# Kernel optimization log

Measured on AMD Instinct MI355X. Metric: run time of the kernel, lower is better.

Reference implementation:

```python
import jax, jax.numpy as jnp
import numpy as np

N_NODES = 300000
DIM = 64
NNZ = 4800000


def setup_inputs() -> dict:
    key = jax.random.key(0)
    ks = jax.random.split(key, 8)
    emb_all = 0.1 * jax.random.normal(ks[0], (N_NODES, DIM), dtype=jnp.float32)
    # edge values ~ symmetric-normalized adjacency scale (avg degree 16 -> ~1/16)
    vals = jax.random.uniform(ks[1], (NNZ,), dtype=jnp.float32) * (1.0 / 16.0)
    vals2 = jax.random.uniform(ks[2], (NNZ,), dtype=jnp.float32) * (1.0 / 16.0)
    rows = jnp.sort(jax.random.randint(ks[3], (NNZ,), 0, N_NODES, dtype=jnp.int32))
    cols = jax.random.randint(ks[4], (NNZ,), 0, N_NODES, dtype=jnp.int32)
    rows2 = jnp.sort(jax.random.randint(ks[5], (NNZ,), 0, N_NODES, dtype=jnp.int32))
    cols2 = jax.random.randint(ks[6], (NNZ,), 0, N_NODES, dtype=jnp.int32)
    return {
        "emb_all": emb_all,
        "vals": vals,
        "vals2": vals2,
        "rows": rows,
        "cols": cols,
        "rows2": rows2,
        "cols2": cols2,
        "n_layers": 3,
        "num_users": 100000,
    }


def _spmm(rows, cols, vals, x, n):
    # sparse [n,n] @ dense [n,d] via gather + segment-sum
    return jax.ops.segment_sum(vals[:, None] * x[cols], rows, num_segments=n)


def _pearson(x, y):
    # per-row pearson correlation over the last (latent) dim -> [N]
    xd = x - jnp.mean(x, axis=-1, keepdims=True)
    yd = y - jnp.mean(y, axis=-1, keepdims=True)
    num = jnp.sum(xd * yd, axis=-1)
    den = jnp.sqrt(jnp.sum(xd * xd, axis=-1)) * jnp.sqrt(jnp.sum(yd * yd, axis=-1))
    den = jnp.where(den < 1e-7, jnp.float32(1e-7), den)
    return num / den


def reference(emb_all, vals, vals2, rows, cols, rows2, cols2, n_layers, num_users):
    n = emb_all.shape[0]
    e0 = emb_all
    embs2 = [e0]
    # layer 0: plain LightGCN propagation on G
    e = _spmm(rows, cols, vals, e0, n)
    embs2.append(e)
    # layers 1..n_layers: pearson-gated propagation on G2
    for _ in range(n_layers):
        b = _pearson(embs2[-1], e0)  # [N]
        prop = _spmm(rows2, cols2, vals2, embs2[-1], n)
        e = b[:, None] * prop + (1.0 - b)[:, None] * e0
        embs2.append(e)
    light_out = jnp.mean(jnp.stack(embs2, axis=1), axis=1)  # [N, d]
    users = light_out[:num_users]
    items = light_out[num_users:]
    return users, items
```

## Files before the change

### kernel.cpp

```cpp
#include <hip/hip_runtime.h>

#define DIM 64

typedef __attribute__((ext_vector_type(4))) float f4;
typedef __attribute__((ext_vector_type(2))) float f2;
typedef __attribute__((ext_vector_type(4))) unsigned int u4;
typedef __attribute__((ext_vector_type(2))) unsigned int u2;

#define SEL_LO 0x01000504u
#define SEL_HI 0x03020706u
#define ONE2   0x3f803f80u

__device__ __forceinline__ float bflo(unsigned u) { return __uint_as_float(u << 16); }
__device__ __forceinline__ float bfhi(unsigned u) { return __uint_as_float(u & 0xffff0000u); }
__device__ __forceinline__ unsigned bfr(float f) {
    unsigned u = __float_as_uint(f);
    return (u + 0x7fffu + ((u >> 16) & 1u)) >> 16;
}
__device__ __forceinline__ unsigned packbf(float e, float o) { return bfr(e) | (bfr(o) << 16); }
__device__ __forceinline__ unsigned cvtpk(float lo, float hi) {
    unsigned r;
    asm("v_cvt_pk_bf16_f32 %0, %1, %2" : "=v"(r) : "v"(lo), "v"(hi));
    return r;
}
__device__ __forceinline__ float dot2bf(unsigned a, unsigned b, float c) {
    float d;
    asm("v_dot2_f32_bf16 %0, %1, %2, %3" : "=v"(d) : "v"(a), "v"(b), "v"(c));
    return d;
}
__device__ __forceinline__ float gsum8(float v) {
    v += __shfl_xor(v, 1, 64);
    v += __shfl_xor(v, 2, 64);
    v += __shfl_xor(v, 4, 64);
    return v;
}

__global__ void build_row_ptr_kernel(const int* __restrict__ rows, int nnz,
                                     int n, int* __restrict__ row_ptr) {
    int r = blockIdx.x * blockDim.x + threadIdx.x;
    if (r > n) return;
    int lo = 0, hi = nnz;
    while (lo < hi) {
        int mid = (lo + hi) >> 1;
        if (rows[mid] < r) lo = mid + 1; else hi = mid;
    }
    row_ptr[r] = lo;
}

__global__ void cvt_bf16_kernel(const float* __restrict__ in,
                                unsigned int* __restrict__ out, int n8) {
    int i = blockIdx.x * blockDim.x + threadIdx.x;
    if (i >= n8) return;
    const f4* p = (const f4*)in + 2 * (size_t)i;
    f4 a = p[0], b = p[1];
    u4 o;
    o.x = packbf(a.x, a.y); o.y = packbf(a.z, a.w);
    o.z = packbf(b.x, b.y); o.w = packbf(b.z, b.w);
    ((u4*)out)[i] = o;
}

template <int MODE>
__global__ __launch_bounds__(256) void layer_kernel(
    const float* __restrict__ emb,
    const unsigned short* __restrict__ t0,
    const unsigned short* __restrict__ eprev,
    const float* __restrict__ vals, const int* __restrict__ cols,
    const int* __restrict__ rp, int n,
    unsigned short* __restrict__ enew,
    const unsigned short* __restrict__ e1t,
    const unsigned short* __restrict__ e2t,
    f2* __restrict__ stats,
    float* __restrict__ out)
{
    const int tid  = threadIdx.x;
    const int lane = tid & 63;
    const int j    = lane & 7;
    const int wave = blockIdx.x * (blockDim.x >> 6) + (tid >> 6);
    const int rowg = wave * 8 + (lane >> 3);
    const int rg   = rowg < n ? rowg : n - 1;

    const int start = rp[rg];
    const int end   = rp[rg + 1];
    const int len   = (rowg < n) ? (end - start) : 0;
    const int b0    = start & ~1;
    const int doff  = b0 - start;

    int ml = len;
    ml = max(ml, __shfl_xor(ml, 8, 64));
    ml = max(ml, __shfl_xor(ml, 16, 64));
    ml = max(ml, __shfl_xor(ml, 32, 64));
    const int steps = (ml + 4) >> 2;

    const char* tb8 = (const char*)eprev;
    const unsigned joff = (unsigned)(j << 4);

    float acc[8] = {0.f, 0.f, 0.f, 0.f, 0.f, 0.f, 0.f, 0.f};

    for (int s = 0; s < steps; ++s) {
        const int k = b0 + (s << 2);
        u2 c01 = *(const u2*)(cols + k);
        u2 c23 = *(const u2*)(cols + k + 2);
        f2 v01 = *(const f2*)(vals + k);
        f2 v23 = *(const f2*)(vals + k + 2);
        const int rel = (s << 2) + doff;
        bool ok0 = (unsigned)(rel)     < (unsigned)len;
        bool ok1 = (unsigned)(rel + 1) < (unsigned)len;
        bool ok2 = (unsigned)(rel + 2) < (unsigned)len;
        bool ok3 = (unsigned)(rel + 3) < (unsigned)len;
        unsigned cc0 = ok0 ? (unsigned)c01.x : 0u;
        unsigned cc1 = ok1 ? (unsigned)c01.y : 0u;
        unsigned cc2 = ok2 ? (unsigned)c23.x : 0u;
        unsigned cc3 = ok3 ? (unsigned)c23.y : 0u;
        float w0 = ok0 ? v01.x : 0.f;
        float w1 = ok1 ? v01.y : 0.f;
        float w2 = ok2 ? v23.x : 0.f;
        float w3 = ok3 ? v23.y : 0.f;
        unsigned vp01 = cvtpk(w0, w1);
        unsigned vp23 = cvtpk(w2, w3);
        u4 g0 = *(const u4*)(tb8 + ((cc0 << 7) + joff));
        u4 g1 = *(const u4*)(tb8 + ((cc1 << 7) + joff));
        u4 g2 = *(const u4*)(tb8 + ((cc2 << 7) + joff));
        u4 g3 = *(const u4*)(tb8 + ((cc3 << 7) + joff));
        acc[0] = dot2bf(__builtin_amdgcn_perm(g0.x, g1.x, SEL_LO), vp01, acc[0]);
        acc[1] = dot2bf(__builtin_amdgcn_perm(g0.x, g1.x, SEL_HI), vp01, acc[1]);
        acc[2] = dot2bf(__builtin_amdgcn_perm(g0.y, g1.y, SEL_LO), vp01, acc[2]);
        acc[3] = dot2bf(__builtin_amdgcn_perm(g0.y, g1.y, SEL_HI), vp01, acc[3]);
        acc[4] = dot2bf(__builtin_amdgcn_perm(g0.z, g1.z, SEL_LO), vp01, acc[4]);
        acc[5] = dot2bf(__builtin_amdgcn_perm(g0.z, g1.z, SEL_HI), vp01, acc[5]);
        acc[6] = dot2bf(__builtin_amdgcn_perm(g0.w, g1.w, SEL_LO), vp01, acc[6]);
        acc[7] = dot2bf(__builtin_amdgcn_perm(g0.w, g1.w, SEL_HI), vp01, acc[7]);
        acc[0] = dot2bf(__builtin_amdgcn_perm(g2.x, g3.x, SEL_LO), vp23, acc[0]);
        acc[1] = dot2bf(__builtin_amdgcn_perm(g2.x, g3.x, SEL_HI), vp23, acc[1]);
        acc[2] = dot2bf(__builtin_amdgcn_perm(g2.y, g3.y, SEL_LO), vp23, acc[2]);
        acc[3] = dot2bf(__builtin_amdgcn_perm(g2.y, g3.y, SEL_HI), vp23, acc[3]);
        acc[4] = dot2bf(__builtin_amdgcn_perm(g2.z, g3.z, SEL_LO), vp23, acc[4]);
        acc[5] = dot2bf(__builtin_amdgcn_perm(g2.z, g3.z, SEL_HI), vp23, acc[5]);
        acc[6] = dot2bf(__builtin_amdgcn_perm(g2.w, g3.w, SEL_LO), vp23, acc[6]);
        acc[7] = dot2bf(__builtin_amdgcn_perm(g2.w, g3.w, SEL_HI), vp23, acc[7]);
    }

    const size_t ro = (size_t)rg << 6;

    if (MODE == 0) {
        u4 yr = *((const u4*)(t0 + ro) + j);
        float sy  = dot2bf(yr.x, ONE2,
                    dot2bf(yr.y, ONE2, dot2bf(yr.z, ONE2, dot2bf(yr.w, ONE2, 0.f))));
        float syy = dot2bf(yr.x, yr.x,
                    dot2bf(yr.y, yr.y, dot2bf(yr.z, yr.z, dot2bf(yr.w, yr.w, 0.f))));
        sy = gsum8(sy); syy = gsum8(syy);
        float my  = sy * (1.f / 64.f);
        float vy  = syy - sy * my;
        float svy = sqrtf(fmaxf(vy, 0.f));
        if (rowg < n) {
            if (j == 0) { f2 st; st.x = my; st.y = svy; stats[rowg] = st; }
            u4 o;
            o.x = cvtpk(acc[0], acc[1]); o.y = cvtpk(acc[2], acc[3]);
            o.z = cvtpk(acc[4], acc[5]); o.w = cvtpk(acc[6], acc[7]);
            *((u4*)(enew + ro) + j) = o;
        }
        return;
    }

    u4 xr = *((const u4*)(eprev + ro) + j);
    u4 yr = *((const u4*)(t0 + ro) + j);
    float sx  = dot2bf(xr.x, ONE2,
                dot2bf(xr.y, ONE2, dot2bf(xr.z, ONE2, dot2bf(xr.w, ONE2, 0.f))));
    float sxx = dot2bf(xr.x, xr.x,
                dot2bf(xr.y, xr.y, dot2bf(xr.z, xr.z, dot2bf(xr.w, xr.w, 0.f))));
    float sxy = dot2bf(xr.x, yr.x,
                dot2bf(xr.y, yr.y, dot2bf(xr.z, yr.z, dot2bf(xr.w, yr.w, 0.f))));
    sx = gsum8(sx); sxx = gsum8(sxx); sxy = gsum8(sxy);

    f2 st = stats[rg];
    float mx  = sx * (1.f / 64.f);
    float num = sxy - sx * st.x;
    float vx  = sxx - sx * mx;
    float den = sqrtf(fmaxf(vx, 0.f)) * st.y;
    den = fmaxf(den, 1e-7f);
    float b  = num / den;
    float ob = 1.f - b;

    if (MODE == 1) {
        float y0[8] = { bflo(yr.x), bfhi(yr.x), bflo(yr.y), bfhi(yr.y),
                        bflo(yr.z), bfhi(yr.z), bflo(yr.w), bfhi(yr.w) };
        if (rowg < n) {
            u4 o;
            o.x = cvtpk(b * acc[0] + ob * y0[0], b * acc[1] + ob * y0[1]);
            o.y = cvtpk(b * acc[2] + ob * y0[2], b * acc[3] + ob * y0[3]);
            o.z = cvtpk(b * acc[4] + ob * y0[4], b * acc[5] + ob * y0[5]);
            o.w = cvtpk(b * acc[6] + ob * y0[6], b * acc[7] + ob * y0[7]);
            *((u4*)(enew + ro) + j) = o;
        }
    } else {
        const f4* ep = (const f4*)(emb + ro) + 2 * j;
        f4 ea = ep[0], eb = ep[1];
        float y0[8] = { ea.x, ea.y, ea.z, ea.w, eb.x, eb.y, eb.z, eb.w };
        float xp[8] = { bflo(xr.x), bfhi(xr.x), bflo(xr.y), bfhi(xr.y),
                        bflo(xr.z), bfhi(xr.z), bflo(xr.w), bfhi(xr.w) };
        u4 r1 = *((const u4*)(e1t + ro) + j);
        u4 r2 = *((const u4*)(e2t + ro) + j);
        float s[8];
        s[0] = y0[0] + bflo(r1.x) + bflo(r2.x) + xp[0] + (b * acc[0] + ob * y0[0]);
        s[1] = y0[1] + bfhi(r1.x) + bfhi(r2.x) + xp[1] + (b * acc[1] + ob * y0[1]);
        s[2] = y0[2] + bflo(r1.y) + bflo(r2.y) + xp[2] + (b * acc[2] + ob * y0[2]);
        s[3] = y0[3] + bfhi(r1.y) + bfhi(r2.y) + xp[3] + (b * acc[3] + ob * y0[3]);
        s[4] = y0[4] + bflo(r1.z) + bflo(r2.z) + xp[4] + (b * acc[4] + ob * y0[4]);
        s[5] = y0[5] + bfhi(r1.z) + bfhi(r2.z) + xp[5] + (b * acc[5] + ob * y0[5]);
        s[6] = y0[6] + bflo(r1.w) + bflo(r2.w) + xp[6] + (b * acc[6] + ob * y0[6]);
        s[7] = y0[7] + bfhi(r1.w) + bfhi(r2.w) + xp[7] + (b * acc[7] + ob * y0[7]);
        if (rowg < n) {
            f4 o0 = { s[0] * 0.2f, s[1] * 0.2f, s[2] * 0.2f, s[3] * 0.2f };
            f4 o1 = { s[4] * 0.2f, s[5] * 0.2f, s[6] * 0.2f, s[7] * 0.2f };
            f4* op = (f4*)(out + ro) + 2 * j;
            op[0] = o0; op[1] = o1;
        }
    }
}

extern "C" void kernel_launch(void* const* d_in, const int* in_sizes, int n_in,
                              void* d_out, int out_size, void* d_ws, size_t ws_size,
                              hipStream_t stream) {
    const float* emb   = (const float*)d_in[0];
    const float* vals  = (const float*)d_in[1];
    const float* vals2 = (const float*)d_in[2];
    const int*   rows  = (const int*)d_in[3];
    const int*   cols  = (const int*)d_in[4];
    const int*   rows2 = (const int*)d_in[5];
    const int*   cols2 = (const int*)d_in[6];

    const int n    = in_sizes[0] / DIM;
    const int nnz  = in_sizes[1];
    const int nnz2 = in_sizes[2];

    float* out = (float*)d_out;

    char*  ws       = (char*)d_ws;
    size_t rp_bytes = (((size_t)(n + 1) * sizeof(int)) + 255) & ~(size_t)255;
    size_t st_bytes = (((size_t)n * sizeof(f2)) + 255) & ~(size_t)255;
    size_t tb_bytes = (size_t)n * DIM * sizeof(unsigned short);
    int* rp1 = (int*)ws;
    int* rp2 = (int*)(ws + rp_bytes);
    f2*  ST  = (f2*)(ws + 2 * rp_bytes);
    unsigned short* T0 = (unsigned short*)(ws + 2 * rp_bytes + st_bytes);
    unsigned short* E1 = (unsigned short*)((char*)T0 + tb_bytes);
    unsigned short* E2 = (unsigned short*)((char*)E1 + tb_bytes);
    unsigned short* E3 = (unsigned short*)((char*)E2 + tb_bytes);

    const int tb = 256;
    build_row_ptr_kernel<<<(n + 1 + tb - 1) / tb, tb, 0, stream>>>(rows,  nnz,  n, rp1);
    build_row_ptr_kernel<<<(n + 1 + tb - 1) / tb, tb, 0, stream>>>(rows2, nnz2, n, rp2);

    const int n8 = n * DIM / 8;
    cvt_bf16_kernel<<<(n8 + tb - 1) / tb, tb, 0, stream>>>(emb, (unsigned int*)T0, n8);

    const int waves = (n + 7) / 8;
    const int grid  = (waves + 3) / 4;
    layer_kernel<0><<<grid, tb, 0, stream>>>(emb, T0, T0, vals, cols, rp1, n,
                                             E1, T0, T0, ST, out);
    layer_kernel<1><<<grid, tb, 0, stream>>>(emb, T0, E1, vals2, cols2, rp2, n,
                                             E2, T0, T0, ST, out);
    layer_kernel<1><<<grid, tb, 0, stream>>>(emb, T0, E2, vals2, cols2, rp2, n,
                                             E3, T0, T0, ST, out);
    layer_kernel<2><<<grid, tb, 0, stream>>>(emb, T0, E3, vals2, cols2, rp2, n,
                                             E3, E1, E2, ST, out);
}
```

Before: 496.3 us.

## Precompute next-layer Pearson coefficient in producer epilogue; unroll gather loop to eight edges

Each layer kernel now computes the Pearson gate for the next layer from its freshly written output row and stores it in a small per-row buffer. Consumer kernels then read one float instead of re-reading the previous row and reducing it, which removes a dependent load and a reduction from the epilogue. The edge loop is also unrolled from four to eight edges per step, with eight row gathers in flight, and the cols/vals stream is read with nontemporal loads. The wider unroll raises register pressure and wastes more padded work on short rows.

Result: slower. 509.2 us (+2.6%).

```diff
diff --git a/kernel.cpp b/kernel.cpp
--- a/kernel.cpp
+++ b/kernel.cpp
@@ -69,7 +69,7 @@
     unsigned short* __restrict__ enew,
     const unsigned short* __restrict__ e1t,
     const unsigned short* __restrict__ e2t,
-    f2* __restrict__ stats,
+    f2* __restrict__ stats, float* __restrict__ bbuf,
     float* __restrict__ out)
 {
     const int tid  = threadIdx.x;
@@ -89,60 +89,85 @@
     ml = max(ml, __shfl_xor(ml, 8, 64));
     ml = max(ml, __shfl_xor(ml, 16, 64));
     ml = max(ml, __shfl_xor(ml, 32, 64));
-    const int steps = (ml + 4) >> 2;
+    const int steps = (ml + 8) >> 3;
 
     const char* tb8 = (const char*)eprev;
     const unsigned joff = (unsigned)(j << 4);
+    const size_t ro = (size_t)rg << 6;
+
+    float bcoef = 0.f;
+    if (MODE != 0) bcoef = bbuf[rg];
+    u4 yr = {};
+    if (MODE != 2) yr = *((const u4*)(t0 + ro) + j);
+    f2 st = {};
+    if (MODE == 1) st = stats[rg];
 
     float acc[8] = {0.f, 0.f, 0.f, 0.f, 0.f, 0.f, 0.f, 0.f};
 
     for (int s = 0; s < steps; ++s) {
-        const int k = b0 + (s << 2);
-        u2 c01 = *(const u2*)(cols + k);
-        u2 c23 = *(const u2*)(cols + k + 2);
-        f2 v01 = *(const f2*)(vals + k);
-        f2 v23 = *(const f2*)(vals + k + 2);
-        const int rel = (s << 2) + doff;
+        const int k = b0 + (s << 3);
+        u2 c01 = __builtin_nontemporal_load((const u2*)(cols + k));
+        u2 c23 = __builtin_nontemporal_load((const u2*)(cols + k + 2));
+        u2 c45 = __builtin_nontemporal_load((const u2*)(cols + k + 4));
+        u2 c67 = __builtin_nontemporal_load((const u2*)(cols + k + 6));
+        f2 v01 = __builtin_nontemporal_load((const f2*)(vals + k));
+        f2 v23 = __builtin_nontemporal_load((const f2*)(vals + k + 2));
+        f2 v45 = __builtin_nontemporal_load((const f2*)(vals + k + 4));
+        f2 v67 = __builtin_nontemporal_load((const f2*)(vals + k + 6));
+        const int rel = (s << 3) + doff;
         bool ok0 = (unsigned)(rel)     < (unsigned)len;
         bool ok1 = (unsigned)(rel + 1) < (unsigned)len;
         bool ok2 = (unsigned)(rel + 2) < (unsigned)len;
         bool ok3 = (unsigned)(rel + 3) < (unsigned)len;
+        bool ok4 = (unsigned)(rel + 4) < (unsigned)len;
+        bool ok5 = (unsigned)(rel + 5) < (unsigned)len;
+        bool ok6 = (unsigned)(rel + 6) < (unsigned)len;
+        bool ok7 = (unsigned)(rel + 7) < (unsigned)len;
         unsigned cc0 = ok0 ? (unsigned)c01.x : 0u;
         unsigned cc1 = ok1 ? (unsigned)c01.y : 0u;
         unsigned cc2 = ok2 ? (unsigned)c23.x : 0u;
         unsigned cc3 = ok3 ? (unsigned)c23.y : 0u;
+        unsigned cc4 = ok4 ? (unsigned)c45.x : 0u;
+        unsigned cc5 = ok5 ? (unsigned)c45.y : 0u;
+        unsigned cc6 = ok6 ? (unsigned)c67.x : 0u;
+        unsigned cc7 = ok7 ? (unsigned)c67.y : 0u;
+        u4 g0 = *(const u4*)(tb8 + ((cc0 << 7) + joff));
+        u4 g1 = *(const u4*)(tb8 + ((cc1 << 7) + joff));
+        u4 g2 = *(const u4*)(tb8 + ((cc2 << 7) + joff));
+        u4 g3 = *(const u4*)(tb8 + ((cc3 << 7) + joff));
+        u4 g4 = *(const u4*)(tb8 + ((cc4 << 7) + joff));
+        u4 g5 = *(const u4*)(tb8 + ((cc5 << 7) + joff));
+        u4 g6 = *(const u4*)(tb8 + ((cc6 << 7) + joff));
+        u4 g7 = *(const u4*)(tb8 + ((cc7 << 7) + joff));
         float w0 = ok0 ? v01.x : 0.f;
         float w1 = ok1 ? v01.y : 0.f;
         float w2 = ok2 ? v23.x : 0.f;
         float w3 = ok3 ? v23.y : 0.f;
+        float w4 = ok4 ? v45.x : 0.f;
+        float w5 = ok5 ? v45.y : 0.f;
+        float w6 = ok6 ? v67.x : 0.f;
+        float w7 = ok7 ? v67.y : 0.f;
         unsigned vp01 = cvtpk(w0, w1);
         unsigned vp23 = cvtpk(w2, w3);
-        u4 g0 = *(const u4*)(tb8 + ((cc0 << 7) + joff));
-        u4 g1 = *(const u4*)(tb8 + ((cc1 << 7) + joff));
-        u4 g2 = *(const u4*)(tb8 + ((cc2 << 7) + joff));
-        u4 g3 = *(const u4*)(tb8 + ((cc3 << 7) + joff));
-        acc[0] = dot2bf(__builtin_amdgcn_perm(g0.x, g1.x, SEL_LO), vp01, acc[0]);
-        acc[1] = dot2bf(__builtin_amdgcn_perm(g0.x, g1.x, SEL_HI), vp01, acc[1]);
-        acc[2] = dot2bf(__builtin_amdgcn_perm(g0.y, g1.y, SEL_LO), vp01, acc[2]);
-        acc[3] = dot2bf(__builtin_amdgcn_perm(g0.y, g1.y, SEL_HI), vp01, acc[3]);
-        acc[4] = dot2bf(__builtin_amdgcn_perm(g0.z, g1.z, SEL_LO), vp01, acc[4]);
-        acc[5] = dot2bf(__builtin_amdgcn_perm(g0.z, g1.z, SEL_HI), vp01, acc[5]);
-        acc[6] = dot2bf(__builtin_amdgcn_perm(g0.w, g1.w, SEL_LO), vp01, acc[6]);
-        acc[7] = dot2bf(__builtin_amdgcn_perm(g0.w, g1.w, SEL_HI), vp01, acc[7]);
-        acc[0] = dot2bf(__builtin_amdgcn_perm(g2.x, g3.x, SEL_LO), vp23, acc[0]);
-        acc[1] = dot2bf(__builtin_amdgcn_perm(g2.x, g3.x, SEL_HI), vp23, acc[1]);
-        acc[2] = dot2bf(__builtin_amdgcn_perm(g2.y, g3.y, SEL_LO), vp23, acc[2]);
-        acc[3] = dot2bf(__builtin_amdgcn_perm(g2.y, g3.y, SEL_HI), vp23, acc[3]);
-        acc[4] = dot2bf(__builtin_amdgcn_perm(g2.z, g3.z, SEL_LO), vp23, acc[4]);
-        acc[5] = dot2bf(__builtin_amdgcn_perm(g2.z, g3.z, SEL_HI), vp23, acc[5]);
-        acc[6] = dot2bf(__builtin_amdgcn_perm(g2.w, g3.w, SEL_LO), vp23, acc[6]);
-        acc[7] = dot2bf(__builtin_amdgcn_perm(g2.w, g3.w, SEL_HI), vp23, acc[7]);
+        unsigned vp45 = cvtpk(w4, w5);
+        unsigned vp67 = cvtpk(w6, w7);
+#define CONSUME(ga, gb, vp)                                                    \
+        acc[0] = dot2bf(__builtin_amdgcn_perm(ga.x, gb.x, SEL_LO), vp, acc[0]);\
+        acc[1] = dot2bf(__builtin_amdgcn_perm(ga.x, gb.x, SEL_HI), vp, acc[1]);\
+        acc[2] = dot2bf(__builtin_amdgcn_perm(ga.y, gb.y, SEL_LO), vp, acc[2]);\
+        acc[3] = dot2bf(__builtin_amdgcn_perm(ga.y, gb.y, SEL_HI), vp, acc[3]);\
+        acc[4] = dot2bf(__builtin_amdgcn_perm(ga.z, gb.z, SEL_LO), vp, acc[4]);\
+        acc[5] = dot2bf(__builtin_amdgcn_perm(ga.z, gb.z, SEL_HI), vp, acc[5]);\
+        acc[6] = dot2bf(__builtin_amdgcn_perm(ga.w, gb.w, SEL_LO), vp, acc[6]);\
+        acc[7] = dot2bf(__builtin_amdgcn_perm(ga.w, gb.w, SEL_HI), vp, acc[7]);
+        CONSUME(g0, g1, vp01)
+        CONSUME(g2, g3, vp23)
+        CONSUME(g4, g5, vp45)
+        CONSUME(g6, g7, vp67)
+#undef CONSUME
     }
 
-    const size_t ro = (size_t)rg << 6;
-
     if (MODE == 0) {
-        u4 yr = *((const u4*)(t0 + ro) + j);
         float sy  = dot2bf(yr.x, ONE2,
                     dot2bf(yr.y, ONE2, dot2bf(yr.z, ONE2, dot2bf(yr.w, ONE2, 0.f))));
         float syy = dot2bf(yr.x, yr.x,
@@ -151,63 +176,78 @@
         float my  = sy * (1.f / 64.f);
         float vy  = syy - sy * my;
         float svy = sqrtf(fmaxf(vy, 0.f));
+        u4 o;
+        o.x = cvtpk(acc[0], acc[1]); o.y = cvtpk(acc[2], acc[3]);
+        o.z = cvtpk(acc[4], acc[5]); o.w = cvtpk(acc[6], acc[7]);
+        float sx  = dot2bf(o.x, ONE2,
+                    dot2bf(o.y, ONE2, dot2bf(o.z, ONE2, dot2bf(o.w, ONE2, 0.f))));
+        float sxx = dot2bf(o.x, o.x,
+                    dot2bf(o.y, o.y, dot2bf(o.z, o.z, dot2bf(o.w, o.w, 0.f))));
+        float sxy = dot2bf(o.x, yr.x,
+                    dot2bf(o.y, yr.y, dot2bf(o.z, yr.z, dot2bf(o.w, yr.w, 0.f))));
+        sx = gsum8(sx); sxx = gsum8(sxx); sxy = gsum8(sxy);
+        float mx  = sx * (1.f / 64.f);
+        float num = sxy - sx * my;
+        float vx  = sxx - sx * mx;
+        float den = sqrtf(fmaxf(vx, 0.f)) * svy;
+        den = fmaxf(den, 1e-7f);
+        float bn = num / den;
         if (rowg < n) {
-            if (j == 0) { f2 st; st.x = my; st.y = svy; stats[rowg] = st; }
-            u4 o;
-            o.x = cvtpk(acc[0], acc[1]); o.y = cvtpk(acc[2], acc[3]);
-            o.z = cvtpk(acc[4], acc[5]); o.w = cvtpk(acc[6], acc[7]);
+            if (j == 0) {
+                f2 s2; s2.x = my; s2.y = svy;
+                stats[rowg] = s2;
+                bbuf[rowg]  = bn;
+            }
             *((u4*)(enew + ro) + j) = o;
         }
         return;
     }
 
-    u4 xr = *((const u4*)(eprev + ro) + j);
-    u4 yr = *((const u4*)(t0 + ro) + j);
-    float sx  = dot2bf(xr.x, ONE2,
-                dot2bf(xr.y, ONE2, dot2bf(xr.z, ONE2, dot2bf(xr.w, ONE2, 0.f))));
-    float sxx = dot2bf(xr.x, xr.x,
-                dot2bf(xr.y, xr.y, dot2bf(xr.z, xr.z, dot2bf(xr.w, xr.w, 0.f))));
-    float sxy = dot2bf(xr.x, yr.x,
-                dot2bf(xr.y, yr.y, dot2bf(xr.z, yr.z, dot2bf(xr.w, yr.w, 0.f))));
-    sx = gsum8(sx); sxx = gsum8(sxx); sxy = gsum8(sxy);
-
-    f2 st = stats[rg];
-    float mx  = sx * (1.f / 64.f);
-    float num = sxy - sx * st.x;
-    float vx  = sxx - sx * mx;
-    float den = sqrtf(fmaxf(vx, 0.f)) * st.y;
-    den = fmaxf(den, 1e-7f);
-    float b  = num / den;
-    float ob = 1.f - b;
+    const float ob = 1.f - bcoef;
 
     if (MODE == 1) {
         float y0[8] = { bflo(yr.x), bfhi(yr.x), bflo(yr.y), bfhi(yr.y),
                         bflo(yr.z), bfhi(yr.z), bflo(yr.w), bfhi(yr.w) };
+        u4 o;
+        o.x = cvtpk(bcoef * acc[0] + ob * y0[0], bcoef * acc[1] + ob * y0[1]);
+        o.y = cvtpk(bcoef * acc[2] + ob * y0[2], bcoef * acc[3] + ob * y0[3]);
+        o.z = cvtpk(bcoef * acc[4] + ob * y0[4], bcoef * acc[5] + ob * y0[5]);
+        o.w = cvtpk(bcoef * acc[6] + ob * y0[6], bcoef * acc[7] + ob * y0[7]);
+        float sx  = dot2bf(o.x, ONE2,
+                    dot2bf(o.y, ONE2, dot2bf(o.z, ONE2, dot2bf(o.w, ONE2, 0.f))));
+        float sxx = dot2bf(o.x, o.x,
+                    dot2bf(o.y, o.y, dot2bf(o.z, o.z, dot2bf(o.w, o.w, 0.f))));
+        float sxy = dot2bf(o.x, yr.x,
+                    dot2bf(o.y, yr.y, dot2bf(o.z, yr.z, dot2bf(o.w, yr.w, 0.f))));
+        sx = gsum8(sx); sxx = gsum8(sxx); sxy = gsum8(sxy);
+        float mx  = sx * (1.f / 64.f);
+        float num = sxy - sx * st.x;
+        float vx  = sxx - sx * mx;
+        float den = sqrtf(fmaxf(vx, 0.f)) * st.y;
+        den = fmaxf(den, 1e-7f);
+        float bn = num / den;
         if (rowg < n) {
-            u4 o;
-            o.x = cvtpk(b * acc[0] + ob * y0[0], b * acc[1] + ob * y0[1]);
-            o.y = cvtpk(b * acc[2] + ob * y0[2], b * acc[3] + ob * y0[3]);
-            o.z = cvtpk(b * acc[4] + ob * y0[4], b * acc[5] + ob * y0[5]);
-            o.w = cvtpk(b * acc[6] + ob * y0[6], b * acc[7] + ob * y0[7]);
+            if (j == 0) bbuf[rowg] = bn;
             *((u4*)(enew + ro) + j) = o;
         }
     } else {
         const f4* ep = (const f4*)(emb + ro) + 2 * j;
         f4 ea = ep[0], eb = ep[1];
         float y0[8] = { ea.x, ea.y, ea.z, ea.w, eb.x, eb.y, eb.z, eb.w };
+        u4 xr = *((const u4*)(eprev + ro) + j);
         float xp[8] = { bflo(xr.x), bfhi(xr.x), bflo(xr.y), bfhi(xr.y),
                         bflo(xr.z), bfhi(xr.z), bflo(xr.w), bfhi(xr.w) };
         u4 r1 = *((const u4*)(e1t + ro) + j);
         u4 r2 = *((const u4*)(e2t + ro) + j);
         float s[8];
-        s[0] = y0[0] + bflo(r1.x) + bflo(r2.x) + xp[0] + (b * acc[0] + ob * y0[0]);
-        s[1] = y0[1] + bfhi(r1.x) + bfhi(r2.x) + xp[1] + (b * acc[1] + ob * y0[1]);
-        s[2] = y0[2] + bflo(r1.y) + bflo(r2.y) + xp[2] + (b * acc[2] + ob * y0[2]);
-        s[3] = y0[3] + bfhi(r1.y) + bfhi(r2.y) + xp[3] + (b * acc[3] + ob * y0[3]);
-        s[4] = y0[4] + bflo(r1.z) + bflo(r2.z) + xp[4] + (b * acc[4] + ob * y0[4]);
-        s[5] = y0[5] + bfhi(r1.z) + bfhi(r2.z) + xp[5] + (b * acc[5] + ob * y0[5]);
-        s[6] = y0[6] + bflo(r1.w) + bflo(r2.w) + xp[6] + (b * acc[6] + ob * y0[6]);
-        s[7] = y0[7] + bfhi(r1.w) + bfhi(r2.w) + xp[7] + (b * acc[7] + ob * y0[7]);
+        s[0] = y0[0] + bflo(r1.x) + bflo(r2.x) + xp[0] + (bcoef * acc[0] + ob * y0[0]);
+        s[1] = y0[1] + bfhi(r1.x) + bfhi(r2.x) + xp[1] + (bcoef * acc[1] + ob * y0[1]);
+        s[2] = y0[2] + bflo(r1.y) + bflo(r2.y) + xp[2] + (bcoef * acc[2] + ob * y0[2]);
+        s[3] = y0[3] + bfhi(r1.y) + bfhi(r2.y) + xp[3] + (bcoef * acc[3] + ob * y0[3]);
+        s[4] = y0[4] + bflo(r1.z) + bflo(r2.z) + xp[4] + (bcoef * acc[4] + ob * y0[4]);
+        s[5] = y0[5] + bfhi(r1.z) + bfhi(r2.z) + xp[5] + (bcoef * acc[5] + ob * y0[5]);
+        s[6] = y0[6] + bflo(r1.w) + bflo(r2.w) + xp[6] + (bcoef * acc[6] + ob * y0[6]);
+        s[7] = y0[7] + bfhi(r1.w) + bfhi(r2.w) + xp[7] + (bcoef * acc[7] + ob * y0[7]);
         if (rowg < n) {
             f4 o0 = { s[0] * 0.2f, s[1] * 0.2f, s[2] * 0.2f, s[3] * 0.2f };
             f4 o1 = { s[4] * 0.2f, s[5] * 0.2f, s[6] * 0.2f, s[7] * 0.2f };
@@ -237,11 +277,13 @@
     char*  ws       = (char*)d_ws;
     size_t rp_bytes = (((size_t)(n + 1) * sizeof(int)) + 255) & ~(size_t)255;
     size_t st_bytes = (((size_t)n * sizeof(f2)) + 255) & ~(size_t)255;
+    size_t bb_bytes = (((size_t)n * sizeof(float)) + 255) & ~(size_t)255;
     size_t tb_bytes = (size_t)n * DIM * sizeof(unsigned short);
-    int* rp1 = (int*)ws;
-    int* rp2 = (int*)(ws + rp_bytes);
-    f2*  ST  = (f2*)(ws + 2 * rp_bytes);
-    unsigned short* T0 = (unsigned short*)(ws + 2 * rp_bytes + st_bytes);
+    int*   rp1 = (int*)ws;
+    int*   rp2 = (int*)(ws + rp_bytes);
+    f2*    ST  = (f2*)(ws + 2 * rp_bytes);
+    float* BB  = (float*)(ws + 2 * rp_bytes + st_bytes);
+    unsigned short* T0 = (unsigned short*)(ws + 2 * rp_bytes + st_bytes + bb_bytes);
     unsigned short* E1 = (unsigned short*)((char*)T0 + tb_bytes);
     unsigned short* E2 = (unsigned short*)((char*)E1 + tb_bytes);
     unsigned short* E3 = (unsigned short*)((char*)E2 + tb_bytes);
@@ -256,11 +298,11 @@
     const int waves = (n + 7) / 8;
     const int grid  = (waves + 3) / 4;
     layer_kernel<0><<<grid, tb, 0, stream>>>(emb, T0, T0, vals, cols, rp1, n,
-                                             E1, T0, T0, ST, out);
+                                             E1, T0, T0, ST, BB, out);
     layer_kernel<1><<<grid, tb, 0, stream>>>(emb, T0, E1, vals2, cols2, rp2, n,
-                                             E2, T0, T0, ST, out);
+                                             E2, T0, T0, ST, BB, out);
     layer_kernel<1><<<grid, tb, 0, stream>>>(emb, T0, E2, vals2, cols2, rp2, n,
-                                             E3, T0, T0, ST, out);
+                                             E3, T0, T0, ST, BB, out);
     layer_kernel<2><<<grid, tb, 0, stream>>>(emb, T0, E3, vals2, cols2, rp2, n,
-                                             E3, E1, E2, ST, out);
-}
+                                             E3, E1, E2, ST, BB, out);
+}
```
